# Kernel tuning notes

Measured on AMD Instinct MI355X. Metric: run time of the kernel, lower is better.

## Reference

```python
import jax, jax.numpy as jnp
import numpy as np

N_NODES = 50000
N_EDGES = 600000
D_FEAT = 128
OUT_DIM = 128


def setup_inputs() -> dict:
    key = jax.random.key(0)
    k1, k2, k3, k4 = jax.random.split(key, 4)
    self_feat = jax.random.normal(k1, (N_NODES, D_FEAT), dtype=jnp.float32)
    nbr_feat = jax.random.normal(k2, (N_EDGES, D_FEAT), dtype=jnp.float32)
    relation_src_indices = jax.random.randint(k3, (N_EDGES,), 0, N_NODES, dtype=jnp.int32)
    # Dense(output_dim, use_bias=False), input dim = 2*D_FEAT due to concat
    W = jax.random.normal(k4, (2 * D_FEAT, OUT_DIM), dtype=jnp.float32) * (1.0 / np.sqrt(2 * D_FEAT))
    return {"self_feat": self_feat, "nbr_feat": nbr_feat,
            "relation_src_indices": relation_src_indices, "W": W}


def reference(self_feat, nbr_feat, relation_src_indices, W):
    num_nodes = self_feat.shape[0]
    # unsorted_segment_mean: sum / count, 0 for empty segments (TF semantics)
    seg_sum = jax.ops.segment_sum(nbr_feat, relation_src_indices, num_segments=num_nodes)
    counts = jax.ops.segment_sum(jnp.ones((nbr_feat.shape[0],), dtype=nbr_feat.dtype),
                                 relation_src_indices, num_segments=num_nodes)
    agg = jnp.where(counts[:, None] > 0, seg_sum / jnp.maximum(counts[:, None], 1.0), 0.0)
    out = jnp.concatenate([self_feat, agg], axis=-1)  # [N, 2*D]
    return out @ W  # [N, OUT_DIM]
```

## Files before the change

### kernel.cpp

```cpp
#include <hip/hip_runtime.h>

#define D 128
#define K2 256

typedef float vfloat4 __attribute__((ext_vector_type(4)));


__global__ void hist_kernel(const int* __restrict__ idx, int* __restrict__ cnt, int n) {
    int e = blockIdx.x * 256 + threadIdx.x;
    if (e < n) atomicAdd(&cnt[idx[e]], 1);
}

__global__ void reduce_kernel(const int* __restrict__ cnt, int* __restrict__ bsum, int n) {
    __shared__ int s[256];
    int i = blockIdx.x * 256 + threadIdx.x;
    s[threadIdx.x] = (i < n) ? cnt[i] : 0;
    __syncthreads();
    for (int d = 128; d > 0; d >>= 1) {
        if (threadIdx.x < d) s[threadIdx.x] += s[threadIdx.x + d];
        __syncthreads();
    }
    if (threadIdx.x == 0) bsum[blockIdx.x] = s[0];
}

__global__ void scan_bsum_kernel(int* __restrict__ bsum, int* __restrict__ off, int nb, int n) {
    __shared__ int s[256];
    int v = (threadIdx.x < nb) ? bsum[threadIdx.x] : 0;
    s[threadIdx.x] = v;
    __syncthreads();
    for (int d = 1; d < 256; d <<= 1) {
        int t = (threadIdx.x >= d) ? s[threadIdx.x - d] : 0;
        __syncthreads();
        s[threadIdx.x] += t;
        __syncthreads();
    }
    if (threadIdx.x < nb) bsum[threadIdx.x] = s[threadIdx.x] - v;
    if (threadIdx.x == 255) off[n] = s[255];
}

__global__ void scan_kernel(const int* __restrict__ cnt, const int* __restrict__ bsum,
                            int* __restrict__ off, int* __restrict__ cur, int n) {
    __shared__ int s[256];
    int i = blockIdx.x * 256 + threadIdx.x;
    int v = (i < n) ? cnt[i] : 0;
    s[threadIdx.x] = v;
    __syncthreads();
    for (int d = 1; d < 256; d <<= 1) {
        int t = (threadIdx.x >= d) ? s[threadIdx.x - d] : 0;
        __syncthreads();
        s[threadIdx.x] += t;
        __syncthreads();
    }
    if (i < n) {
        int e = bsum[blockIdx.x] + s[threadIdx.x] - v;
        off[i] = e;
        cur[i] = e;
    }
}

__global__ void scatter_kernel(const int* __restrict__ idx, int* __restrict__ cur,
                               int* __restrict__ eid, int n) {
    int e = blockIdx.x * 256 + threadIdx.x;
    if (e < n) {
        int p = atomicAdd(&cur[idx[e]], 1);
        eid[p] = e;
    }
}


__global__ __launch_bounds__(64) void aggregate_kernel(const float* __restrict__ nbr,
                                                       const int* __restrict__ eid,
                                                       const int* __restrict__ off,
                                                       float* __restrict__ agg) {
    const int node = blockIdx.x;
    const int beg = off[node], end = off[node + 1];
    const int t = threadIdx.x;
    const int h = t >> 5;
    const int l = t & 31;
    const vfloat4* __restrict__ rows = (const vfloat4*)nbr;
    vfloat4 acc = {0.f, 0.f, 0.f, 0.f};
    int j = beg;
    for (; j + 8 <= end; j += 8) {
        int e0 = eid[j + 0 + h];
        int e1 = eid[j + 2 + h];
        int e2 = eid[j + 4 + h];
        int e3 = eid[j + 6 + h];
        vfloat4 v0 = __builtin_nontemporal_load(rows + (size_t)e0 * 32 + l);
        vfloat4 v1 = __builtin_nontemporal_load(rows + (size_t)e1 * 32 + l);
        vfloat4 v2 = __builtin_nontemporal_load(rows + (size_t)e2 * 32 + l);
        vfloat4 v3 = __builtin_nontemporal_load(rows + (size_t)e3 * 32 + l);
        acc += (v0 + v1) + (v2 + v3);
    }
    if (j + 4 <= end) {
        int e0 = eid[j + 0 + h];
        int e1 = eid[j + 2 + h];
        vfloat4 v0 = __builtin_nontemporal_load(rows + (size_t)e0 * 32 + l);
        vfloat4 v1 = __builtin_nontemporal_load(rows + (size_t)e1 * 32 + l);
        acc += v0 + v1;
        j += 4;
    }
    for (; j < end; j += 2) {
        int jj = j + h;
        if (jj < end) {
            int e = eid[jj];
            vfloat4 v = __builtin_nontemporal_load(rows + (size_t)e * 32 + l);
            acc += v;
        }
    }
    acc.x += __shfl_xor(acc.x, 32);
    acc.y += __shfl_xor(acc.y, 32);
    acc.z += __shfl_xor(acc.z, 32);
    acc.w += __shfl_xor(acc.w, 32);
    int c = end - beg;
    float inv = (c > 0) ? 1.0f / (float)c : 0.0f;
    if (h == 0) {
        vfloat4 o = acc * inv;
        *((vfloat4*)agg + (size_t)node * 32 + l) = o;
    }
}


#define MT 64
#define KB 32
#define XP (MT + 4)

__global__ __launch_bounds__(128) void matmul_kernel(const float* __restrict__ self,
                                                     const float* __restrict__ agg,
                                                     const float* __restrict__ W,
                                                     float* __restrict__ out, int nNodes) {
    __shared__ float Xs[KB][XP];
    __shared__ float Ws[KB][D];
    const int t = threadIdx.x;
    const int m_base = blockIdx.x * MT;
    const int n0 = (t & 15) * 8;
    const int m0 = (t >> 4) * 8;

    float acc[8][8];
#pragma unroll
    for (int i = 0; i < 8; ++i)
#pragma unroll
        for (int j = 0; j < 8; ++j) acc[i][j] = 0.f;

    for (int k0 = 0; k0 < K2; k0 += KB) {
        const float* src = (k0 < D) ? self : agg;
        const int koff = k0 & (D - 1);
#pragma unroll
        for (int it = 0; it < 4; ++it) {
            int lin = t + it * 128;
            int row = lin >> 3;
            int k4 = lin & 7;
            int gr = m_base + row;
            if (gr >= nNodes) gr = nNodes - 1;
            float4 v = *(const float4*)(src + (size_t)gr * D + koff + k4 * 4);
            Xs[k4 * 4 + 0][row] = v.x;
            Xs[k4 * 4 + 1][row] = v.y;
            Xs[k4 * 4 + 2][row] = v.z;
            Xs[k4 * 4 + 3][row] = v.w;
        }
#pragma unroll
        for (int it = 0; it < 8; ++it) {
            int lin = t + it * 128;
            int kk = lin >> 5;
            int n4 = lin & 31;
            *(float4*)(&Ws[kk][n4 * 4]) = *(const float4*)(W + (size_t)(k0 + kk) * D + n4 * 4);
        }
        __syncthreads();

#pragma unroll
        for (int kk4 = 0; kk4 < KB / 4; ++kk4) {
            float4 xa[4], xb[4], wa[4], wb[4];
#pragma unroll
            for (int kq = 0; kq < 4; ++kq) {
                int k = kk4 * 4 + kq;
                xa[kq] = *(const float4*)(&Xs[k][m0]);
                xb[kq] = *(const float4*)(&Xs[k][m0 + 4]);
                wa[kq] = *(const float4*)(&Ws[k][n0]);
                wb[kq] = *(const float4*)(&Ws[k][n0 + 4]);
            }
#pragma unroll
            for (int kq = 0; kq < 4; ++kq) {
                const float xr[8] = {xa[kq].x, xa[kq].y, xa[kq].z, xa[kq].w,
                                     xb[kq].x, xb[kq].y, xb[kq].z, xb[kq].w};
                const float wr[8] = {wa[kq].x, wa[kq].y, wa[kq].z, wa[kq].w,
                                     wb[kq].x, wb[kq].y, wb[kq].z, wb[kq].w};
#pragma unroll
                for (int i = 0; i < 8; ++i)
#pragma unroll
                    for (int j = 0; j < 8; ++j) acc[i][j] += xr[i] * wr[j];
            }
        }
        __syncthreads();
    }

#pragma unroll
    for (int i = 0; i < 8; ++i) {
        int gr = m_base + m0 + i;
        if (gr < nNodes) {
            float4 o0 = make_float4(acc[i][0], acc[i][1], acc[i][2], acc[i][3]);
            float4 o1 = make_float4(acc[i][4], acc[i][5], acc[i][6], acc[i][7]);
            *(float4*)(out + (size_t)gr * D + n0) = o0;
            *(float4*)(out + (size_t)gr * D + n0 + 4) = o1;
        }
    }
}


extern "C" void kernel_launch(void* const* d_in, const int* in_sizes, int n_in,
                              void* d_out, int out_size, void* d_ws, size_t ws_size,
                              hipStream_t stream) {
    const float* self = (const float*)d_in[0];
    const float* nbr = (const float*)d_in[1];
    const int* idx = (const int*)d_in[2];
    const float* W = (const float*)d_in[3];
    float* out = (float*)d_out;

    const int nNodes = in_sizes[0] / D;
    const int nEdges = in_sizes[2];
    const int nb = (nNodes + 255) / 256;

    int* cnt = (int*)d_ws;
    int* off = cnt + nNodes;
    int* cur = off + (nNodes + 1);
    int* bsum = cur + nNodes;
    int* eid = bsum + 256;

    hipMemsetAsync(cnt, 0, (size_t)nNodes * sizeof(int), stream);
    hist_kernel<<<(nEdges + 255) / 256, 256, 0, stream>>>(idx, cnt, nEdges);
    reduce_kernel<<<nb, 256, 0, stream>>>(cnt, bsum, nNodes);
    scan_bsum_kernel<<<1, 256, 0, stream>>>(bsum, off, nb, nNodes);
    scan_kernel<<<nb, 256, 0, stream>>>(cnt, bsum, off, cur, nNodes);
    scatter_kernel<<<(nEdges + 255) / 256, 256, 0, stream>>>(idx, cur, eid, nEdges);

    aggregate_kernel<<<nNodes, 64, 0, stream>>>(nbr, eid, off, out);
    matmul_kernel<<<(nNodes + MT - 1) / MT, 128, 0, stream>>>(self, out, W, out, nNodes);
}
```

Before: 532.9 us.

## Use split-bf16 MFMA for the dense projection instead of FP32 FMA

Replaces the scalar FP32 register-tiled matmul with a kernel built on MFMA 16x16x32 bf16 instructions. Both operands are split into high and low bf16 parts, and three products (hh, hl, lh) are accumulated to approximate FP32 accuracy. A new small kernel pre-splits and transposes W into the workspace. The matmul is small next to the gather-bound aggregation, so total gains are limited. Dropping the low-low product adds a small precision risk.

```diff
diff --git a/kernel.cpp b/kernel.cpp
--- a/kernel.cpp
+++ b/kernel.cpp
@@ -4,6 +4,18 @@
 #define K2 256
 
 typedef float vfloat4 __attribute__((ext_vector_type(4)));
+typedef float f32x4 __attribute__((ext_vector_type(4)));
+typedef short bf16x8 __attribute__((ext_vector_type(8)));
+typedef unsigned short ushort8 __attribute__((ext_vector_type(8)));
+
+__device__ __forceinline__ unsigned short f2bf(float f) {
+    unsigned int u = __float_as_uint(f);
+    u += 0x7fffu + ((u >> 16) & 1u);
+    return (unsigned short)(u >> 16);
+}
+__device__ __forceinline__ float bf2f(unsigned short h) {
+    return __uint_as_float((unsigned int)h << 16);
+}
 
 
 __global__ void hist_kernel(const int* __restrict__ idx, int* __restrict__ cnt, int n) {
@@ -65,6 +77,19 @@
         int p = atomicAdd(&cur[idx[e]], 1);
         eid[p] = e;
     }
+}
+
+
+__global__ __launch_bounds__(256) void wsplit_kernel(const float* __restrict__ W,
+                                                     unsigned short* __restrict__ wh,
+                                                     unsigned short* __restrict__ wl) {
+    const int k = threadIdx.x;
+    const int n = blockIdx.x;
+    float x = W[(size_t)k * D + n];
+    unsigned short h = f2bf(x);
+    float lo = x - bf2f(h);
+    wh[(size_t)n * K2 + k] = h;
+    wl[(size_t)n * K2 + k] = f2bf(lo);
 }
 
 
@@ -120,86 +145,98 @@
 }
 
 
-#define MT 64
-#define KB 32
-#define XP (MT + 4)
-
-__global__ __launch_bounds__(128) void matmul_kernel(const float* __restrict__ self,
-                                                     const float* __restrict__ agg,
-                                                     const float* __restrict__ W,
-                                                     float* __restrict__ out, int nNodes) {
-    __shared__ float Xs[KB][XP];
-    __shared__ float Ws[KB][D];
+#define BM 64
+
+__global__ __launch_bounds__(256) void matmul_kernel(const float* __restrict__ self,
+                                                     const float* agg,
+                                                     const unsigned short* __restrict__ whT,
+                                                     const unsigned short* __restrict__ wlT,
+                                                     float* out, int nNodes) {
+    __shared__ alignas(16) unsigned short AhS[BM * 32];
+    __shared__ alignas(16) unsigned short AlS[BM * 32];
+
     const int t = threadIdx.x;
-    const int m_base = blockIdx.x * MT;
-    const int n0 = (t & 15) * 8;
-    const int m0 = (t >> 4) * 8;
-
-    float acc[8][8];
-#pragma unroll
-    for (int i = 0; i < 8; ++i)
-#pragma unroll
-        for (int j = 0; j < 8; ++j) acc[i][j] = 0.f;
-
-    for (int k0 = 0; k0 < K2; k0 += KB) {
+    const int m_base = blockIdx.x * BM;
+
+    const int sr = t >> 2;
+    const int sq = t & 3;
+    const int sp = sq ^ ((sr >> 1) & 3);
+    int gr = m_base + sr;
+    if (gr >= nNodes) gr = nNodes - 1;
+
+    const int wid = t >> 6;
+    const int l = t & 63;
+    const int wm = (wid >> 1) << 5;
+    const int wn = (wid & 1) << 6;
+    const int lr = l & 15;
+    const int g = l >> 4;
+    const int slot = g ^ ((lr >> 1) & 3);
+
+    f32x4 acc[2][4];
+#pragma unroll
+    for (int i = 0; i < 2; ++i)
+#pragma unroll
+        for (int j = 0; j < 4; ++j) acc[i][j] = (f32x4){0.f, 0.f, 0.f, 0.f};
+
+    for (int k0 = 0; k0 < K2; k0 += 32) {
         const float* src = (k0 < D) ? self : agg;
-        const int koff = k0 & (D - 1);
-#pragma unroll
-        for (int it = 0; it < 4; ++it) {
-            int lin = t + it * 128;
-            int row = lin >> 3;
-            int k4 = lin & 7;
-            int gr = m_base + row;
-            if (gr >= nNodes) gr = nNodes - 1;
-            float4 v = *(const float4*)(src + (size_t)gr * D + koff + k4 * 4);
-            Xs[k4 * 4 + 0][row] = v.x;
-            Xs[k4 * 4 + 1][row] = v.y;
-            Xs[k4 * 4 + 2][row] = v.z;
-            Xs[k4 * 4 + 3][row] = v.w;
-        }
-#pragma unroll
-        for (int it = 0; it < 8; ++it) {
-            int lin = t + it * 128;
-            int kk = lin >> 5;
-            int n4 = lin & 31;
-            *(float4*)(&Ws[kk][n4 * 4]) = *(const float4*)(W + (size_t)(k0 + kk) * D + n4 * 4);
-        }
-        __syncthreads();
-
-#pragma unroll
-        for (int kk4 = 0; kk4 < KB / 4; ++kk4) {
-            float4 xa[4], xb[4], wa[4], wb[4];
-#pragma unroll
-            for (int kq = 0; kq < 4; ++kq) {
-                int k = kk4 * 4 + kq;
-                xa[kq] = *(const float4*)(&Xs[k][m0]);
-                xb[kq] = *(const float4*)(&Xs[k][m0 + 4]);
-                wa[kq] = *(const float4*)(&Ws[k][n0]);
-                wb[kq] = *(const float4*)(&Ws[k][n0 + 4]);
+        const float* p = src + (size_t)gr * D + (k0 & (D - 1)) + sq * 8;
+        vfloat4 v0 = ((const vfloat4*)p)[0];
+        vfloat4 v1 = ((const vfloat4*)p)[1];
+        float xs[8] = {v0.x, v0.y, v0.z, v0.w, v1.x, v1.y, v1.z, v1.w};
+        ushort8 hv, lv;
+#pragma unroll
+        for (int i = 0; i < 8; ++i) {
+            unsigned short h = f2bf(xs[i]);
+            hv[i] = h;
+            lv[i] = f2bf(xs[i] - bf2f(h));
+        }
+        *(ushort8*)&AhS[sr * 32 + sp * 8] = hv;
+        *(ushort8*)&AlS[sr * 32 + sp * 8] = lv;
+        __syncthreads();
+
+        bf16x8 bh[4], bl[4], ah[2], al[2];
+#pragma unroll
+        for (int nf = 0; nf < 4; ++nf) {
+            size_t boff = (size_t)(wn + nf * 16 + lr) * K2 + k0 + g * 8;
+            bh[nf] = *(const bf16x8*)(whT + boff);
+            bl[nf] = *(const bf16x8*)(wlT + boff);
+        }
+#pragma unroll
+        for (int mf = 0; mf < 2; ++mf) {
+            int row = wm + mf * 16 + lr;
+            ah[mf] = *(const bf16x8*)&AhS[row * 32 + slot * 8];
+            al[mf] = *(const bf16x8*)&AlS[row * 32 + slot * 8];
+        }
+
+#pragma unroll
+        for (int mf = 0; mf < 2; ++mf)
+#pragma unroll
+            for (int nf = 0; nf < 4; ++nf)
+                acc[mf][nf] = __builtin_amdgcn_mfma_f32_16x16x32_bf16(ah[mf], bh[nf], acc[mf][nf], 0, 0, 0);
+#pragma unroll
+        for (int mf = 0; mf < 2; ++mf)
+#pragma unroll
+            for (int nf = 0; nf < 4; ++nf)
+                acc[mf][nf] = __builtin_amdgcn_mfma_f32_16x16x32_bf16(ah[mf], bl[nf], acc[mf][nf], 0, 0, 0);
+#pragma unroll
+        for (int mf = 0; mf < 2; ++mf)
+#pragma unroll
+            for (int nf = 0; nf < 4; ++nf)
+                acc[mf][nf] = __builtin_amdgcn_mfma_f32_16x16x32_bf16(al[mf], bh[nf], acc[mf][nf], 0, 0, 0);
+        __syncthreads();
+    }
+
+#pragma unroll
+    for (int mf = 0; mf < 2; ++mf) {
+#pragma unroll
+        for (int rr = 0; rr < 4; ++rr) {
+            int m = m_base + wm + mf * 16 + g * 4 + rr;
+            if (m < nNodes) {
+                float* po = out + (size_t)m * D + wn + lr;
+#pragma unroll
+                for (int nf = 0; nf < 4; ++nf) po[nf * 16] = acc[mf][nf][rr];
             }
-#pragma unroll
-            for (int kq = 0; kq < 4; ++kq) {
-                const float xr[8] = {xa[kq].x, xa[kq].y, xa[kq].z, xa[kq].w,
-                                     xb[kq].x, xb[kq].y, xb[kq].z, xb[kq].w};
-                const float wr[8] = {wa[kq].x, wa[kq].y, wa[kq].z, wa[kq].w,
-                                     wb[kq].x, wb[kq].y, wb[kq].z, wb[kq].w};
-#pragma unroll
-                for (int i = 0; i < 8; ++i)
-#pragma unroll
-                    for (int j = 0; j < 8; ++j) acc[i][j] += xr[i] * wr[j];
-            }
-        }
-        __syncthreads();
-    }
-
-#pragma unroll
-    for (int i = 0; i < 8; ++i) {
-        int gr = m_base + m0 + i;
-        if (gr < nNodes) {
-            float4 o0 = make_float4(acc[i][0], acc[i][1], acc[i][2], acc[i][3]);
-            float4 o1 = make_float4(acc[i][4], acc[i][5], acc[i][6], acc[i][7]);
-            *(float4*)(out + (size_t)gr * D + n0) = o0;
-            *(float4*)(out + (size_t)gr * D + n0 + 4) = o1;
         }
     }
 }
@@ -223,8 +260,13 @@
     int* cur = off + (nNodes + 1);
     int* bsum = cur + nNodes;
     int* eid = bsum + 256;
+    size_t csr_bytes = ((size_t)(3 * nNodes + 1 + 256) + (size_t)nEdges) * sizeof(int);
+    csr_bytes = (csr_bytes + 15) & ~(size_t)15;
+    unsigned short* whT = (unsigned short*)((char*)d_ws + csr_bytes);
+    unsigned short* wlT = whT + (size_t)D * K2;
 
     hipMemsetAsync(cnt, 0, (size_t)nNodes * sizeof(int), stream);
+    wsplit_kernel<<<D, K2, 0, stream>>>(W, whT, wlT);
     hist_kernel<<<(nEdges + 255) / 256, 256, 0, stream>>>(idx, cnt, nEdges);
     reduce_kernel<<<nb, 256, 0, stream>>>(cnt, bsum, nNodes);
     scan_bsum_kernel<<<1, 256, 0, stream>>>(bsum, off, nb, nNodes);
@@ -232,5 +274,5 @@
     scatter_kernel<<<(nEdges + 255) / 256, 256, 0, stream>>>(idx, cur, eid, nEdges);
 
     aggregate_kernel<<<nNodes, 64, 0, stream>>>(nbr, eid, off, out);
-    matmul_kernel<<<(nNodes + MT - 1) / MT, 128, 0, stream>>>(self, out, W, out, nNodes);
-}
+    matmul_kernel<<<(nNodes + BM - 1) / BM, 256, 0, stream>>>(self, out, whT, wlT, out, nNodes);
+}
```

Result: faster. 519.0 us (-2.6%).
